# Kernel tuning notes

Hardware: AMD Instinct MI355X
Metric: run time of the kernel (lower is better)

The kernel has to match this reference:

```python
import jax, jax.numpy as jnp
import numpy as np

D, H, E, HID, TOPK = 1024, 16, 8, 2048, 2
B, L = 2, 2048

def setup_inputs() -> dict:
    key = jax.random.key(0)
    ks = jax.random.split(key, 12)
    s = 0.02
    return {
        "x": jax.random.normal(ks[0], (B, L, D), jnp.float32),
        "mask": jnp.zeros((B, L), dtype=bool),  # key_padding_mask: True = ignore
        "ln1_g": jnp.ones((D,), jnp.float32), "ln1_b": jnp.zeros((D,), jnp.float32),
        "Wqkv": jax.random.normal(ks[1], (3 * D, D), jnp.float32) * s,
        "bqkv": jnp.zeros((3 * D,), jnp.float32),
        "Wo": jax.random.normal(ks[2], (D, D), jnp.float32) * s,
        "bo": jnp.zeros((D,), jnp.float32),
        "ln2_g": jnp.ones((D,), jnp.float32), "ln2_b": jnp.zeros((D,), jnp.float32),
        "Wg": jax.random.normal(ks[3], (D, E), jnp.float32) * s,
        "bg": jnp.zeros((E,), jnp.float32),
        "W1": jax.random.normal(ks[4], (E, D, HID), jnp.float32) * s,
        "b1": jnp.zeros((E, HID), jnp.float32),
        "W2": jax.random.normal(ks[5], (E, HID, D), jnp.float32) * s,
        "b2": jnp.zeros((E, D), jnp.float32),
    }

def _layernorm(x, g, b, eps=1e-5):
    mu = x.mean(-1, keepdims=True)
    var = ((x - mu) ** 2).mean(-1, keepdims=True)
    return (x - mu) * jax.lax.rsqrt(var + eps) * g + b

def reference(x, mask, ln1_g, ln1_b, Wqkv, bqkv, Wo, bo, ln2_g, ln2_b, Wg, bg, W1, b1, W2, b2):
    b, l, d = x.shape
    dh = d // H
    # ---- pre-norm self-attention ----
    residual = x
    xn = _layernorm(x, ln1_g, ln1_b)
    qkv = xn @ Wqkv.T + bqkv                      # [B,L,3D]
    q, k, v = jnp.split(qkv, 3, axis=-1)
    q = q.reshape(b, l, H, dh).transpose(0, 2, 1, 3)  # bhld
    k = k.reshape(b, l, H, dh).transpose(0, 2, 1, 3)
    v = v.reshape(b, l, H, dh).transpose(0, 2, 1, 3)
    scores = jnp.einsum('bhqd,bhkd->bhqk', q, k) / jnp.sqrt(jnp.float32(dh))
    scores = jnp.where(mask[:, None, None, :], jnp.float32(-1e9), scores)
    attn = jax.nn.softmax(scores, axis=-1)
    ao = jnp.einsum('bhqk,bhkd->bhqd', attn, v).transpose(0, 2, 1, 3).reshape(b, l, d)
    ao = ao @ Wo.T + bo
    x = residual + ao                              # dropout is identity at eval
    # ---- pre-norm MoE FFN (top-2 softmax gating) ----
    residual = x
    xn = _layernorm(x, ln2_g, ln2_b)
    T = b * l
    xf = xn.reshape(T, d)
    probs = jax.nn.softmax(xf @ Wg + bg, axis=-1)  # [T,E]
    vals, idx = jax.lax.top_k(probs, TOPK)         # [T,K]
    wts = vals / vals.sum(-1, keepdims=True)
    # dense expert compute (reference): all experts over all tokens
    h = jax.nn.gelu(jnp.einsum('td,edh->eth', xf, W1) + b1[:, None, :], approximate=False)
    eo = jnp.einsum('eth,ehd->etd', h, W2) + b2[:, None, :]   # [E,T,D]
    sel = eo[idx, jnp.arange(T)[:, None]]          # [T,K,D]
    moe_out = (wts[..., None] * sel).sum(1).reshape(b, l, d)
    # load-balancing aux loss
    me = probs.mean(0)                             # mean gate prob per expert
    ce = jax.nn.one_hot(idx, E, dtype=probs.dtype).sum(1).mean(0)  # dispatch fraction
    moe_loss = jnp.float32(E) * jnp.sum(me * ce)
    out = residual + moe_out
    return (out, moe_loss)
```

## Files before the change

### kernel.cpp

```cpp
#include <hip/hip_runtime.h>
#include <stdint.h>

#define TOK   4096
#define DIM   1024
#define NH    16
#define DHD   64
#define NE    8
#define HIDN  2048
#define BATCH 2
#define SEQ   2048
#define BK    64

using floatx4 = __attribute__((ext_vector_type(4))) float;
using bfx8    = __attribute__((ext_vector_type(8))) __bf16;
using bfx2    = __attribute__((ext_vector_type(2))) __bf16;
using shortx8 = __attribute__((ext_vector_type(8))) short;

__device__ __forceinline__ unsigned short f2bf(float f) {
    union { __bf16 b; unsigned short u; } v;
    v.b = (__bf16)f;
    return v.u;
}

__device__ __forceinline__ unsigned pack2bf(float lo, float hi) {
    union { bfx2 v; unsigned u; } t;
    t.v[0] = (__bf16)lo;
    t.v[1] = (__bf16)hi;
    return t.u;
}

__device__ __forceinline__ floatx4 mfma16(bfx8 a, bfx8 b, floatx4 c) {
    return __builtin_amdgcn_mfma_f32_16x16x32_bf16(a, b, c, 0, 0, 0);
}

__device__ __forceinline__ void gload16(const unsigned short* g, unsigned short* l) {
    __builtin_amdgcn_global_load_lds(
        (const __attribute__((address_space(1))) unsigned int*)g,
        (__attribute__((address_space(3))) unsigned int*)l, 16, 0, 0);
}

__global__ __launch_bounds__(256) void cvt_kernel(const float* __restrict__ in,
                                                  unsigned short* __restrict__ out, int n) {
    int i = (blockIdx.x * 256 + threadIdx.x) * 4;
    if (i < n) {
        float4 v = *reinterpret_cast<const float4*>(in + i);
        out[i + 0] = f2bf(v.x);
        out[i + 1] = f2bf(v.y);
        out[i + 2] = f2bf(v.z);
        out[i + 3] = f2bf(v.w);
    }
}

__global__ __launch_bounds__(256) void transpose_cvt_kernel(const float* __restrict__ in,
                                                            unsigned short* __restrict__ out,
                                                            int R, int C) {
    __shared__ unsigned short t[64][65];
    in  += (size_t)blockIdx.z * R * C;
    out += (size_t)blockIdx.z * R * C;
    int r0 = blockIdx.y * 64, c0 = blockIdx.x * 64;
    int lr = threadIdx.x >> 4, lc = (threadIdx.x & 15) * 4;
#pragma unroll
    for (int p = 0; p < 4; p++) {
        int r = p * 16 + lr;
        float4 v = *reinterpret_cast<const float4*>(in + (size_t)(r0 + r) * C + c0 + lc);
        t[lc + 0][r] = f2bf(v.x);
        t[lc + 1][r] = f2bf(v.y);
        t[lc + 2][r] = f2bf(v.z);
        t[lc + 3][r] = f2bf(v.w);
    }
    __syncthreads();
    int c = threadIdx.x >> 2, ch = (threadIdx.x & 3) * 16;
    shortx8 o0, o1;
#pragma unroll
    for (int q = 0; q < 8; q++) { o0[q] = t[c][ch + q]; o1[q] = t[c][ch + 8 + q]; }
    unsigned short* op = out + (size_t)(c0 + c) * R + r0 + ch;
    *reinterpret_cast<shortx8*>(op) = o0;
    *reinterpret_cast<shortx8*>(op + 8) = o1;
}

__global__ __launch_bounds__(256) void kvprep_kernel(const unsigned short* __restrict__ qkv,
                                                     unsigned short* __restrict__ ktg,
                                                     unsigned short* __restrict__ vtg,
                                                     const unsigned char* __restrict__ mask,
                                                     float* __restrict__ maskf) {
    __shared__ unsigned short t[64 * 64];
    int tid = threadIdx.x;
    int s0 = blockIdx.x * 64, hd = blockIdx.y, b = blockIdx.z;
    size_t bh = (size_t)(b * NH + hd);
    if (hd == 0 && tid < 64) {
        maskf[(size_t)b * SEQ + s0 + tid] =
            mask[(size_t)b * SEQ + s0 + tid] ? -1.44269504e9f : 0.0f;
    }
#pragma unroll
    for (int i = 0; i < 2; i++) {
        int idx = i * 256 + tid;
        int sr = idx >> 3, c = idx & 7;
        shortx8 v = *reinterpret_cast<const shortx8*>(
            qkv + (size_t)(b * SEQ + s0 + sr) * 3 * DIM + DIM + hd * DHD + c * 8);
        *reinterpret_cast<shortx8*>(ktg + (bh * SEQ + s0 + sr) * DHD + c * 8) = v;
    }
#pragma unroll
    for (int i = 0; i < 2; i++) {
        int idx = i * 256 + tid;
        int sr = idx >> 3, c = idx & 7;
        shortx8 v = *reinterpret_cast<const shortx8*>(
            qkv + (size_t)(b * SEQ + s0 + sr) * 3 * DIM + 2 * DIM + hd * DHD + c * 8);
        *reinterpret_cast<shortx8*>(t + sr * 64 + ((c ^ (sr >> 3)) * 8)) = v;
    }
    __syncthreads();
#pragma unroll
    for (int i = 0; i < 2; i++) {
        int idx = i * 256 + tid;
        int d = idx >> 3, c2 = idx & 7;
        shortx8 o;
#pragma unroll
        for (int e = 0; e < 8; e++) {
            int s = c2 * 8 + e;
            o[e] = (short)t[s * 64 + (((d >> 3) ^ c2) * 8) + (d & 7)];
        }
        *reinterpret_cast<shortx8*>(vtg + (bh * DHD + d) * SEQ + s0 + c2 * 8) = o;
    }
}

__global__ __launch_bounds__(256) void ln_kernel(const float* __restrict__ x,
                                                 const float* __restrict__ g,
                                                 const float* __restrict__ b,
                                                 unsigned short* __restrict__ obf) {
    int t = blockIdx.x;
    int tid = threadIdx.x;
    const float* xr = x + (size_t)t * DIM;
    float4 v = *reinterpret_cast<const float4*>(xr + tid * 4);
    float s  = v.x + v.y + v.z + v.w;
    float s2 = v.x * v.x + v.y * v.y + v.z * v.z + v.w * v.w;
    for (int o = 32; o > 0; o >>= 1) {
        s  += __shfl_down(s,  o, 64);
        s2 += __shfl_down(s2, o, 64);
    }
    __shared__ float red[10];
    int lane = tid & 63, w = tid >> 6;
    if (lane == 0) { red[w] = s; red[4 + w] = s2; }
    __syncthreads();
    if (tid == 0) {
        float ts = red[0] + red[1] + red[2] + red[3];
        float t2 = red[4] + red[5] + red[6] + red[7];
        float mu = ts * (1.0f / DIM);
        float var = t2 * (1.0f / DIM) - mu * mu;
        red[8] = mu;
        red[9] = rsqrtf(var + 1e-5f);
    }
    __syncthreads();
    float mu = red[8], rstd = red[9];
    float4 gv = *reinterpret_cast<const float4*>(g + tid * 4);
    float4 bv = *reinterpret_cast<const float4*>(b + tid * 4);
    size_t o = (size_t)t * DIM + tid * 4;
    obf[o + 0] = f2bf((v.x - mu) * rstd * gv.x + bv.x);
    obf[o + 1] = f2bf((v.y - mu) * rstd * gv.y + bv.y);
    obf[o + 2] = f2bf((v.z - mu) * rstd * gv.z + bv.z);
    obf[o + 3] = f2bf((v.w - mu) * rstd * gv.w + bv.w);
}

template <int EPI, bool GATHER>
__global__ __launch_bounds__(256) void gemm_kernel(const unsigned short* __restrict__ A,
                                                   const unsigned short* __restrict__ Bt,
                                                   void* __restrict__ C,
                                                   const float* __restrict__ bias,
                                                   const float* __restrict__ resid,
                                                   const int* __restrict__ cnt,
                                                   const int* __restrict__ goff,
                                                   const int* __restrict__ gtok,
                                                   int M, int N, int K) {
    int e = blockIdx.z;
    int Me = cnt ? cnt[e] : M;
    int brow = blockIdx.y * 128;
    if (brow >= Me) return;
    int bcol = blockIdx.x * 128;
    int go = goff ? goff[e] : 0;
    const unsigned short* Be = Bt + (size_t)e * N * K;
    const float* biasp = bias + (size_t)e * N;

    __shared__ unsigned short As[128 * BK];
    __shared__ unsigned short Bs[128 * BK];

    int tid = threadIdx.x, lane = tid & 63, w = tid >> 6;
    int wr = w >> 1, wc = w & 1;
    int cg = lane >> 4, cl = lane & 15;

    const unsigned short* aga[4];
    const unsigned short* bga[4];
    unsigned short* asb = As + w * 2048;
    unsigned short* bsb = Bs + w * 2048;
#pragma unroll
    for (int i = 0; i < 4; i++) {
        int s = w * 256 + i * 64 + lane;
        int row = s >> 3;
        int c = (s & 7) ^ (row & 7);
        int gr = brow + row;
        if (gr >= Me) gr = Me - 1;
        long ar;
        if (GATHER) ar = gtok[go + gr];
        else if (cnt) ar = go + gr;
        else ar = gr;
        aga[i] = A + ar * (long)K + c * 8;
        bga[i] = Be + (size_t)(bcol + row) * K + c * 8;
    }

    floatx4 acc[4][4];
#pragma unroll
    for (int m = 0; m < 4; m++)
#pragma unroll
        for (int n = 0; n < 4; n++) acc[m][n] = (floatx4){0.f, 0.f, 0.f, 0.f};

    for (int kt = 0; kt < K; kt += BK) {
#pragma unroll
        for (int i = 0; i < 4; i++) {
            gload16(aga[i], asb + i * 512);
            gload16(bga[i], bsb + i * 512);
            aga[i] += BK;
            bga[i] += BK;
        }
        __syncthreads();
#pragma unroll
        for (int ks = 0; ks < 2; ks++) {
            bfx8 af[4], bf[4];
#pragma unroll
            for (int m = 0; m < 4; m++) {
                int row = wr * 64 + m * 16 + cl;
                af[m] = *reinterpret_cast<const bfx8*>(
                    As + row * BK + (((ks * 4 + cg) ^ (row & 7)) << 3));
            }
#pragma unroll
            for (int n = 0; n < 4; n++) {
                int row = wc * 64 + n * 16 + cl;
                bf[n] = *reinterpret_cast<const bfx8*>(
                    Bs + row * BK + (((ks * 4 + cg) ^ (row & 7)) << 3));
            }
#pragma unroll
            for (int m = 0; m < 4; m++)
#pragma unroll
                for (int n = 0; n < 4; n++) acc[m][n] = mfma16(af[m], bf[n], acc[m][n]);
        }
        __syncthreads();
    }

#pragma unroll
    for (int m = 0; m < 4; m++) {
#pragma unroll
        for (int j = 0; j < 4; j++) {
            int r = brow + wr * 64 + m * 16 + cg * 4 + j;
            if (r >= Me) continue;
#pragma unroll
            for (int n = 0; n < 4; n++) {
                int col = bcol + wc * 64 + n * 16 + cl;
                float v = acc[m][n][j] + biasp[col];
                if (EPI == 0) {
                    ((unsigned short*)C)[(size_t)r * N + col] = f2bf(v);
                } else if (EPI == 1) {
                    size_t o = (size_t)r * N + col;
                    ((float*)C)[o] = v + resid[o];
                } else if (EPI == 2) {
                    float gg = 0.5f * v * (1.0f + erff(v * 0.70710678f));
                    ((unsigned short*)C)[(size_t)(go + r) * N + col] = f2bf(gg);
                } else {
                    ((float*)C)[(size_t)(go + r) * N + col] = v;
                }
            }
        }
    }
}

__global__ __launch_bounds__(256) void attn_kernel(const unsigned short* __restrict__ qkv,
                                                   const unsigned short* __restrict__ ktg,
                                                   const unsigned short* __restrict__ vtg,
                                                   const float* __restrict__ maskf,
                                                   unsigned short* __restrict__ ao) {
    __shared__ unsigned short Ks[2][64 * 64];
    __shared__ unsigned short Vs[2][64 * 64];
    __shared__ unsigned short Ps[4][16 * 72];

    int tid = threadIdx.x, lane = tid & 63, w = tid >> 6;
    int cg = lane >> 4, cl = lane & 15;
    int qb = blockIdx.x * 64, hd = blockIdx.y, b = blockIdx.z;
    size_t bh = (size_t)(b * NH + hd);
    const float SC2 = 0.125f * 1.44269504f;

    int tq = qb + w * 16 + cl;
    const unsigned short* qrow = qkv + (size_t)(b * SEQ + tq) * 3 * DIM + hd * DHD;
    bfx8 aq0 = *reinterpret_cast<const bfx8*>(qrow + cg * 8);
    bfx8 aq1 = *reinterpret_cast<const bfx8*>(qrow + 32 + cg * 8);

    int srow = lane >> 3, schunk = lane & 7;
    int sg = (schunk ^ srow) * 8;
    const unsigned short* kptr = ktg + (bh * SEQ + w * 16 + srow) * DHD + sg;
    const unsigned short* vptr = vtg + (bh * DHD + w * 16 + srow) * SEQ + sg;
    const float* mrowf = maskf + (size_t)b * SEQ;
    unsigned short* psw = &Ps[w][0];
    int sw0 = (cg ^ (cl & 7)) << 3;

    floatx4 accO[4];
#pragma unroll
    for (int dt = 0; dt < 4; dt++) accO[dt] = (floatx4){0.f, 0.f, 0.f, 0.f};
    float m0 = -3.0e38f, l0 = 0.f;

    gload16(kptr, &Ks[0][w * 1024]);
    gload16(kptr + 8 * DHD, &Ks[0][w * 1024 + 512]);
    gload16(vptr, &Vs[0][w * 1024]);
    gload16(vptr + 8 * SEQ, &Vs[0][w * 1024 + 512]);
    __syncthreads();

    int cur = 0;
    for (int t = 0; t < SEQ / 64; t++) {
        if (t < SEQ / 64 - 1) {
            size_t nkt = (size_t)(t + 1) * 64;
            int nb = cur ^ 1;
            gload16(kptr + nkt * DHD, &Ks[nb][w * 1024]);
            gload16(kptr + nkt * DHD + 8 * DHD, &Ks[nb][w * 1024 + 512]);
            gload16(vptr + nkt, &Vs[nb][w * 1024]);
            gload16(vptr + nkt + 8 * SEQ, &Vs[nb][w * 1024 + 512]);
        }
        const unsigned short* ksb = &Ks[cur][0];
        const unsigned short* vsb = &Vs[cur][0];
        int kt = t * 64;

        floatx4 accS[4];
#pragma unroll
        for (int nt = 0; nt < 4; nt++) accS[nt] = (floatx4){0.f, 0.f, 0.f, 0.f};
#pragma unroll
        for (int nt = 0; nt < 4; nt++) {
            const unsigned short* kr = ksb + (nt * 16 + cl) * 64;
            bfx8 k0 = *reinterpret_cast<const bfx8*>(kr + sw0);
            bfx8 k1 = *reinterpret_cast<const bfx8*>(kr + (sw0 ^ 32));
            accS[nt] = mfma16(k0, aq0, accS[nt]);
            accS[nt] = mfma16(k1, aq1, accS[nt]);
        }

        float s[4][4];
        float tmax = -3.0e38f;
#pragma unroll
        for (int nt = 0; nt < 4; nt++) {
            float4 mk4 = *reinterpret_cast<const float4*>(mrowf + kt + nt * 16 + cg * 4);
            s[nt][0] = fmaf(accS[nt][0], SC2, mk4.x);
            s[nt][1] = fmaf(accS[nt][1], SC2, mk4.y);
            s[nt][2] = fmaf(accS[nt][2], SC2, mk4.z);
            s[nt][3] = fmaf(accS[nt][3], SC2, mk4.w);
#pragma unroll
            for (int j = 0; j < 4; j++) tmax = fmaxf(tmax, s[nt][j]);
        }
        tmax = fmaxf(tmax, __shfl_xor(tmax, 16, 64));
        tmax = fmaxf(tmax, __shfl_xor(tmax, 32, 64));

        if (!__all(tmax - m0 <= 11.5f)) {
            float mn = fmaxf(m0, tmax);
            float al = __builtin_amdgcn_exp2f(m0 - mn);
            m0 = mn;
            l0 *= al;
#pragma unroll
            for (int dt = 0; dt < 4; dt++) accO[dt] *= al;
        }

        float rs = 0.f;
        unsigned pk[4][2];
#pragma unroll
        for (int nt = 0; nt < 4; nt++) {
            float p0 = __builtin_amdgcn_exp2f(s[nt][0] - m0);
            float p1 = __builtin_amdgcn_exp2f(s[nt][1] - m0);
            float p2 = __builtin_amdgcn_exp2f(s[nt][2] - m0);
            float p3 = __builtin_amdgcn_exp2f(s[nt][3] - m0);
            rs += (p0 + p1) + (p2 + p3);
            pk[nt][0] = pack2bf(p0, p1);
            pk[nt][1] = pack2bf(p2, p3);
        }
        rs += __shfl_xor(rs, 16, 64);
        rs += __shfl_xor(rs, 32, 64);
        l0 += rs;

#pragma unroll
        for (int nt = 0; nt < 4; nt++) {
            uint2 u; u.x = pk[nt][0]; u.y = pk[nt][1];
            *reinterpret_cast<uint2*>(psw + cl * 72 + nt * 16 + cg * 4) = u;
        }
        bfx8 pf0 = *reinterpret_cast<const bfx8*>(psw + cl * 72 + cg * 8);
        bfx8 pf1 = *reinterpret_cast<const bfx8*>(psw + cl * 72 + 32 + cg * 8);
#pragma unroll
        for (int dt = 0; dt < 4; dt++) {
            const unsigned short* vr = vsb + (dt * 16 + cl) * 64;
            bfx8 v0 = *reinterpret_cast<const bfx8*>(vr + sw0);
            bfx8 v1 = *reinterpret_cast<const bfx8*>(vr + (sw0 ^ 32));
            accO[dt] = mfma16(v0, pf0, accO[dt]);
            accO[dt] = mfma16(v1, pf1, accO[dt]);
        }
        __syncthreads();
        cur ^= 1;
    }

    float rl = 1.0f / l0;
    unsigned short* aorow = ao + (size_t)(b * SEQ + qb + w * 16 + cl) * DIM + hd * DHD;
#pragma unroll
    for (int dt = 0; dt < 4; dt++) {
        uint2 u;
        u.x = pack2bf(accO[dt][0] * rl, accO[dt][1] * rl);
        u.y = pack2bf(accO[dt][2] * rl, accO[dt][3] * rl);
        *reinterpret_cast<uint2*>(aorow + dt * 16 + cg * 4) = u;
    }
}

__global__ __launch_bounds__(256) void gate_kernel(const float* __restrict__ x2,
                                                   const float* __restrict__ lng,
                                                   const float* __restrict__ lnb,
                                                   const float* __restrict__ Wg,
                                                   const float* __restrict__ bg,
                                                   unsigned short* __restrict__ xn2b,
                                                   int* __restrict__ idx,
                                                   float* __restrict__ wts,
                                                   float* __restrict__ me_part) {
    __shared__ float bme[8];
    if (threadIdx.x < 8) bme[threadIdx.x] = 0.f;
    __syncthreads();
    int w = threadIdx.x >> 6, lane = threadIdx.x & 63;
    int t = blockIdx.x * 4 + w;
    const float* xr = x2 + (size_t)t * DIM + lane * 16;
    float4 xv[4];
    float s = 0.f, s2 = 0.f;
#pragma unroll
    for (int q = 0; q < 4; q++) {
        xv[q] = *reinterpret_cast<const float4*>(xr + q * 4);
        s  += xv[q].x + xv[q].y + xv[q].z + xv[q].w;
        s2 += xv[q].x * xv[q].x + xv[q].y * xv[q].y + xv[q].z * xv[q].z + xv[q].w * xv[q].w;
    }
    for (int o = 32; o > 0; o >>= 1) {
        s  += __shfl_xor(s,  o, 64);
        s2 += __shfl_xor(s2, o, 64);
    }
    float mu = s * (1.0f / DIM);
    float rstd = rsqrtf(s2 * (1.0f / DIM) - mu * mu + 1e-5f);
    float acc[8];
#pragma unroll
    for (int e = 0; e < 8; e++) acc[e] = 0.f;
    unsigned short ob[16];
#pragma unroll
    for (int q = 0; q < 4; q++) {
        float4 gv = *reinterpret_cast<const float4*>(lng + lane * 16 + q * 4);
        float4 bv = *reinterpret_cast<const float4*>(lnb + lane * 16 + q * 4);
        float xn0 = (xv[q].x - mu) * rstd * gv.x + bv.x;
        float xn1 = (xv[q].y - mu) * rstd * gv.y + bv.y;
        float xn2 = (xv[q].z - mu) * rstd * gv.z + bv.z;
        float xn3 = (xv[q].w - mu) * rstd * gv.w + bv.w;
        ob[q * 4 + 0] = f2bf(xn0);
        ob[q * 4 + 1] = f2bf(xn1);
        ob[q * 4 + 2] = f2bf(xn2);
        ob[q * 4 + 3] = f2bf(xn3);
        const float* wr = Wg + (size_t)(lane * 16 + q * 4) * 8;
#pragma unroll
        for (int e = 0; e < 8; e++) acc[e] += xn0 * wr[e];
#pragma unroll
        for (int e = 0; e < 8; e++) acc[e] += xn1 * wr[8 + e];
#pragma unroll
        for (int e = 0; e < 8; e++) acc[e] += xn2 * wr[16 + e];
#pragma unroll
        for (int e = 0; e < 8; e++) acc[e] += xn3 * wr[24 + e];
    }
    unsigned short* op = xn2b + (size_t)t * DIM + lane * 16;
    *reinterpret_cast<shortx8*>(op)     = *reinterpret_cast<shortx8*>(&ob[0]);
    *reinterpret_cast<shortx8*>(op + 8) = *reinterpret_cast<shortx8*>(&ob[8]);
    for (int o = 32; o > 0; o >>= 1)
#pragma unroll
        for (int e = 0; e < 8; e++) acc[e] += __shfl_xor(acc[e], o, 64);
    if (lane == 0) {
        float p[8];
        float mx = -3e38f;
#pragma unroll
        for (int e = 0; e < 8; e++) { acc[e] += bg[e]; mx = fmaxf(mx, acc[e]); }
        float se = 0.f;
#pragma unroll
        for (int e = 0; e < 8; e++) { p[e] = expf(acc[e] - mx); se += p[e]; }
#pragma unroll
        for (int e = 0; e < 8; e++) p[e] /= se;
        int i0 = 0; float v0 = p[0];
#pragma unroll
        for (int e = 1; e < 8; e++) if (p[e] > v0) { v0 = p[e]; i0 = e; }
        int i1 = -1; float v1 = -3e38f;
#pragma unroll
        for (int e = 0; e < 8; e++) if (e != i0 && p[e] > v1) { v1 = p[e]; i1 = e; }
        float sw = v0 + v1;
        idx[t * 2]     = i0;
        idx[t * 2 + 1] = i1;
        wts[t * 2]     = v0 / sw;
        wts[t * 2 + 1] = v1 / sw;
#pragma unroll
        for (int e = 0; e < 8; e++) atomicAdd(&bme[e], p[e]);
    }
    __syncthreads();
    if (threadIdx.x < 8) me_part[(size_t)blockIdx.x * 8 + threadIdx.x] = bme[threadIdx.x];
}

__global__ __launch_bounds__(256) void route1_kernel(const int* __restrict__ idx,
                                                     int* __restrict__ cnt,
                                                     int* __restrict__ posl) {
    __shared__ int lh[8];
    __shared__ int gb[8];
    int tid = threadIdx.x;
    int t = blockIdx.x * 256 + tid;
    if (tid < 8) lh[tid] = 0;
    __syncthreads();
    int i0 = idx[t * 2], i1 = idx[t * 2 + 1];
    int r0 = atomicAdd(&lh[i0], 1);
    int r1 = atomicAdd(&lh[i1], 1);
    __syncthreads();
    if (tid < 8) gb[tid] = atomicAdd(&cnt[tid], lh[tid]);
    __syncthreads();
    posl[t * 2]     = gb[i0] + r0;
    posl[t * 2 + 1] = gb[i1] + r1;
}

__global__ void prefix_kernel(const int* __restrict__ cnt, int* __restrict__ goff) {
    if (threadIdx.x == 0) {
        int s = 0;
        for (int e = 0; e < 8; e++) { goff[e] = s; s += cnt[e]; }
        goff[8] = s;
    }
}

__global__ __launch_bounds__(256) void route2_kernel(const int* __restrict__ idx,
                                                     const int* __restrict__ goff,
                                                     const int* __restrict__ posl,
                                                     int* __restrict__ gtok,
                                                     int* __restrict__ tpos) {
    int t = blockIdx.x * 256 + threadIdx.x;
#pragma unroll
    for (int j = 0; j < 2; j++) {
        int e = idx[t * 2 + j];
        int p = goff[e] + posl[t * 2 + j];
        gtok[p] = t;
        tpos[t * 2 + j] = p;
    }
}

__global__ __launch_bounds__(256) void combine_kernel(const float* __restrict__ x2,
                                                      const float* __restrict__ eo,
                                                      const float* __restrict__ wts,
                                                      const int* __restrict__ tpos,
                                                      float* __restrict__ out) {
    int t = blockIdx.x;
    int c = threadIdx.x * 4;
    float w0 = wts[t * 2], w1 = wts[t * 2 + 1];
    int p0 = tpos[t * 2], p1 = tpos[t * 2 + 1];
    float4 r  = *reinterpret_cast<const float4*>(x2 + (size_t)t * DIM + c);
    float4 a  = *reinterpret_cast<const float4*>(eo + (size_t)p0 * DIM + c);
    float4 bb = *reinterpret_cast<const float4*>(eo + (size_t)p1 * DIM + c);
    float4 o;
    o.x = r.x + w0 * a.x + w1 * bb.x;
    o.y = r.y + w0 * a.y + w1 * bb.y;
    o.z = r.z + w0 * a.z + w1 * bb.z;
    o.w = r.w + w0 * a.w + w1 * bb.w;
    *reinterpret_cast<float4*>(out + (size_t)t * DIM + c) = o;
}

__global__ __launch_bounds__(256) void loss_kernel(const float* __restrict__ me_part,
                                                   const int* __restrict__ cnt,
                                                   float* __restrict__ out) {
    __shared__ float red[256];
    int tid = threadIdx.x;
    int e = tid & 7, part = tid >> 3;
    float s = 0.f;
    for (int b = part; b < 1024; b += 32) s += me_part[(size_t)b * 8 + e];
    red[tid] = s;
    __syncthreads();
    if (tid < 64) {
        float v = red[tid] + red[tid + 64] + red[tid + 128] + red[tid + 192];
        red[tid] = v;
    }
    __syncthreads();
    if (tid < 8) {
        float v = red[tid] + red[tid + 8] + red[tid + 16] + red[tid + 24] +
                  red[tid + 32] + red[tid + 40] + red[tid + 48] + red[tid + 56];
        red[tid] = v;
    }
    __syncthreads();
    if (tid == 0) {
        float s2 = 0.f;
        for (int ee = 0; ee < 8; ee++)
            s2 += (red[ee] / 4096.0f) * ((float)cnt[ee] / 4096.0f);
        out[(size_t)TOK * DIM] = 8.0f * s2;
    }
}

extern "C" void kernel_launch(void* const* d_in, const int* in_sizes, int n_in,
                              void* d_out, int out_size, void* d_ws, size_t ws_size,
                              hipStream_t stream) {
    const float* x    = (const float*)d_in[0];
    const unsigned char* mask = (const unsigned char*)d_in[1];
    const float* ln1g = (const float*)d_in[2];
    const float* ln1b = (const float*)d_in[3];
    const float* Wqkv = (const float*)d_in[4];
    const float* bqkv = (const float*)d_in[5];
    const float* Wo   = (const float*)d_in[6];
    const float* bo   = (const float*)d_in[7];
    const float* ln2g = (const float*)d_in[8];
    const float* ln2b = (const float*)d_in[9];
    const float* Wg   = (const float*)d_in[10];
    const float* bg   = (const float*)d_in[11];
    const float* W1   = (const float*)d_in[12];
    const float* b1   = (const float*)d_in[13];
    const float* W2   = (const float*)d_in[14];
    const float* b2   = (const float*)d_in[15];
    float* out = (float*)d_out;

    char* ws = (char*)d_ws;
    int*   cnt  = (int*)(ws + 0);
    int*   goff = (int*)(ws + 128);
    size_t off = 1024;
    auto alloc = [&](size_t bytes) -> void* {
        void* p = ws + off;
        off += (bytes + 255) & ~(size_t)255;
        return p;
    };
    const size_t SZ_QKVB = (size_t)TOK * 3 * DIM * 2;
    const size_t SZ_HB   = (size_t)2 * TOK * HIDN * 2;
    const size_t SZ_EOF  = (size_t)2 * TOK * DIM * 4;
    char* R1 = (char*)alloc(SZ_HB > SZ_QKVB ? SZ_HB : SZ_QKVB);
    char* R2 = (char*)alloc(SZ_EOF);
    unsigned short* qkvb  = (unsigned short*)R1;
    unsigned short* hb    = (unsigned short*)R1;
    float*          eof   = (float*)R2;
    unsigned short* xn1   = (unsigned short*)R2;
    unsigned short* aob   = (unsigned short*)(R2 + (size_t)TOK * DIM * 2);
    unsigned short* wqkvb = (unsigned short*)(R2 + (size_t)2 * TOK * DIM * 2);
    unsigned short* wob   = (unsigned short*)(R2 + (size_t)2 * TOK * DIM * 2 +
                                              (size_t)3 * DIM * DIM * 2);
    float*          x2    = (float*)alloc((size_t)TOK * DIM * 4);
    unsigned short* xn2b  = (unsigned short*)alloc((size_t)TOK * DIM * 2);
    unsigned short* w1t   = (unsigned short*)alloc((size_t)NE * DIM * HIDN * 2);
    unsigned short* w2t   = (unsigned short*)alloc((size_t)NE * DIM * HIDN * 2);
    unsigned short* ktg   = (unsigned short*)alloc((size_t)BATCH * NH * SEQ * DHD * 2);
    unsigned short* vtg   = (unsigned short*)alloc((size_t)BATCH * NH * DHD * SEQ * 2);
    float*          maskf = (float*)alloc((size_t)BATCH * SEQ * 4);
    float*          mep   = (float*)alloc((size_t)1024 * 8 * 4);
    int*            idxp  = (int*)alloc((size_t)TOK * 2 * 4);
    float*          wtsp  = (float*)alloc((size_t)TOK * 2 * 4);
    int*            posl  = (int*)alloc((size_t)TOK * 2 * 4);
    int*            gtok  = (int*)alloc((size_t)2 * TOK * 4);
    int*            tpos  = (int*)alloc((size_t)TOK * 2 * 4);

    hipMemsetAsync(ws, 0, 256, stream);

    cvt_kernel<<<3 * DIM * DIM / 1024, 256, 0, stream>>>(Wqkv, wqkvb, 3 * DIM * DIM);
    cvt_kernel<<<DIM * DIM / 1024, 256, 0, stream>>>(Wo, wob, DIM * DIM);
    transpose_cvt_kernel<<<dim3(HIDN / 64, DIM / 64, NE), 256, 0, stream>>>(W1, w1t, DIM, HIDN);
    transpose_cvt_kernel<<<dim3(DIM / 64, HIDN / 64, NE), 256, 0, stream>>>(W2, w2t, HIDN, DIM);

    ln_kernel<<<TOK, 256, 0, stream>>>(x, ln1g, ln1b, xn1);

    gemm_kernel<0, false><<<dim3(24, 32, 1), 256, 0, stream>>>(
        xn1, wqkvb, qkvb, bqkv, nullptr, nullptr, nullptr, nullptr, TOK, 3 * DIM, DIM);

    kvprep_kernel<<<dim3(SEQ / 64, NH, BATCH), 256, 0, stream>>>(qkvb, ktg, vtg, mask, maskf);

    attn_kernel<<<dim3(SEQ / 64, NH, BATCH), 256, 0, stream>>>(qkvb, ktg, vtg, maskf, aob);

    gemm_kernel<1, false><<<dim3(8, 32, 1), 256, 0, stream>>>(
        aob, wob, x2, bo, x, nullptr, nullptr, nullptr, TOK, DIM, DIM);

    gate_kernel<<<TOK / 4, 256, 0, stream>>>(x2, ln2g, ln2b, Wg, bg, xn2b,
                                             idxp, wtsp, mep);
    route1_kernel<<<TOK / 256, 256, 0, stream>>>(idxp, cnt, posl);
    prefix_kernel<<<1, 64, 0, stream>>>(cnt, goff);
    route2_kernel<<<TOK / 256, 256, 0, stream>>>(idxp, goff, posl, gtok, tpos);

    gemm_kernel<2, true><<<dim3(16, 32, 8), 256, 0, stream>>>(
        xn2b, w1t, hb, b1, nullptr, cnt, goff, gtok, TOK, HIDN, DIM);

    gemm_kernel<3, false><<<dim3(8, 32, 8), 256, 0, stream>>>(
        hb, w2t, eof, b2, nullptr, cnt, goff, nullptr, TOK, DIM, HIDN);

    combine_kernel<<<TOK, 256, 0, stream>>>(x2, eof, wtsp, tpos, out);
    loss_kernel<<<1, 256, 0, stream>>>(mep, cnt, out);
}
```

Measured before the change: 403.1 us.

## Process two query tiles per attention wave and XCD-swizzle GEMM block order

Each attention wave now handles 32 query rows (two 16-row tiles) instead of 16, so every K/V tile loaded into shared memory serves twice as many queries and the grid is halved. The softmax rescale check is evaluated per lane before the cross-lane max shuffles, so the shuffles run only when a rescale is needed. The GEMM kernel remaps its flattened block index so that consecutive logical tiles land on the same XCD, aiming for better L2 reuse. The cost is higher register pressure in attention (launch bounds now request 2 blocks per SM) and fewer attention blocks to spread across CUs.

New measurement: 366.6 us. 1.1x faster.

```diff
diff --git a/kernel.cpp b/kernel.cpp
--- a/kernel.cpp
+++ b/kernel.cpp
@@ -37,6 +37,12 @@
     __builtin_amdgcn_global_load_lds(
         (const __attribute__((address_space(1))) unsigned int*)g,
         (__attribute__((address_space(3))) unsigned int*)l, 16, 0, 0);
+}
+
+__device__ __forceinline__ int xcd_swz(int hw, int nwg) {
+    int q = nwg >> 3, r = nwg & 7;
+    int xc = hw & 7, o = hw >> 3;
+    return (xc < r ? xc * (q + 1) : r * (q + 1) + (xc - r) * q) + o;
 }
 
 __global__ __launch_bounds__(256) void cvt_kernel(const float* __restrict__ in,
@@ -169,11 +175,19 @@
                                                    const int* __restrict__ goff,
                                                    const int* __restrict__ gtok,
                                                    int M, int N, int K) {
-    int e = blockIdx.z;
+    int gx = gridDim.x, gy = gridDim.y;
+    int nwg = gx * gy * (int)gridDim.z;
+    int hw = ((int)blockIdx.z * gy + (int)blockIdx.y) * gx + (int)blockIdx.x;
+    int virt = xcd_swz(hw, nwg);
+    int bx = virt % gx;
+    int tmp = virt / gx;
+    int by = tmp % gy;
+    int e = tmp / gy;
+
     int Me = cnt ? cnt[e] : M;
-    int brow = blockIdx.y * 128;
+    int brow = by * 128;
     if (brow >= Me) return;
-    int bcol = blockIdx.x * 128;
+    int bcol = bx * 128;
     int go = goff ? goff[e] : 0;
     const unsigned short* Be = Bt + (size_t)e * N * K;
     const float* biasp = bias + (size_t)e * N;
@@ -268,38 +282,46 @@
     }
 }
 
-__global__ __launch_bounds__(256) void attn_kernel(const unsigned short* __restrict__ qkv,
-                                                   const unsigned short* __restrict__ ktg,
-                                                   const unsigned short* __restrict__ vtg,
-                                                   const float* __restrict__ maskf,
-                                                   unsigned short* __restrict__ ao) {
+__global__ __launch_bounds__(256, 2) void attn_kernel(const unsigned short* __restrict__ qkv,
+                                                      const unsigned short* __restrict__ ktg,
+                                                      const unsigned short* __restrict__ vtg,
+                                                      const float* __restrict__ maskf,
+                                                      unsigned short* __restrict__ ao) {
     __shared__ unsigned short Ks[2][64 * 64];
     __shared__ unsigned short Vs[2][64 * 64];
-    __shared__ unsigned short Ps[4][16 * 72];
+    __shared__ unsigned short Ps[4][2][16 * 72];
 
     int tid = threadIdx.x, lane = tid & 63, w = tid >> 6;
     int cg = lane >> 4, cl = lane & 15;
-    int qb = blockIdx.x * 64, hd = blockIdx.y, b = blockIdx.z;
+    int qb = blockIdx.x * 128, hd = blockIdx.y, b = blockIdx.z;
     size_t bh = (size_t)(b * NH + hd);
     const float SC2 = 0.125f * 1.44269504f;
 
-    int tq = qb + w * 16 + cl;
-    const unsigned short* qrow = qkv + (size_t)(b * SEQ + tq) * 3 * DIM + hd * DHD;
-    bfx8 aq0 = *reinterpret_cast<const bfx8*>(qrow + cg * 8);
-    bfx8 aq1 = *reinterpret_cast<const bfx8*>(qrow + 32 + cg * 8);
+    const unsigned short* qrow0 =
+        qkv + (size_t)(b * SEQ + qb + w * 32 + cl) * 3 * DIM + hd * DHD;
+    const unsigned short* qrow1 = qrow0 + (size_t)16 * 3 * DIM;
+    bfx8 aq00 = *reinterpret_cast<const bfx8*>(qrow0 + cg * 8);
+    bfx8 aq01 = *reinterpret_cast<const bfx8*>(qrow0 + 32 + cg * 8);
+    bfx8 aq10 = *reinterpret_cast<const bfx8*>(qrow1 + cg * 8);
+    bfx8 aq11 = *reinterpret_cast<const bfx8*>(qrow1 + 32 + cg * 8);
 
     int srow = lane >> 3, schunk = lane & 7;
     int sg = (schunk ^ srow) * 8;
     const unsigned short* kptr = ktg + (bh * SEQ + w * 16 + srow) * DHD + sg;
     const unsigned short* vptr = vtg + (bh * DHD + w * 16 + srow) * SEQ + sg;
     const float* mrowf = maskf + (size_t)b * SEQ;
-    unsigned short* psw = &Ps[w][0];
+    unsigned short* psw0 = &Ps[w][0][0];
+    unsigned short* psw1 = &Ps[w][1][0];
     int sw0 = (cg ^ (cl & 7)) << 3;
 
-    floatx4 accO[4];
-#pragma unroll
-    for (int dt = 0; dt < 4; dt++) accO[dt] = (floatx4){0.f, 0.f, 0.f, 0.f};
-    float m0 = -3.0e38f, l0 = 0.f;
+    floatx4 accO0[4], accO1[4];
+#pragma unroll
+    for (int dt = 0; dt < 4; dt++) {
+        accO0[dt] = (floatx4){0.f, 0.f, 0.f, 0.f};
+        accO1[dt] = (floatx4){0.f, 0.f, 0.f, 0.f};
+    }
+    float m00 = -3.0e38f, l00 = 0.f;
+    float m01 = -3.0e38f, l01 = 0.f;
 
     gload16(kptr, &Ks[0][w * 1024]);
     gload16(kptr + 8 * DHD, &Ks[0][w * 1024 + 512]);
@@ -321,85 +343,139 @@
         const unsigned short* vsb = &Vs[cur][0];
         int kt = t * 64;
 
-        floatx4 accS[4];
-#pragma unroll
-        for (int nt = 0; nt < 4; nt++) accS[nt] = (floatx4){0.f, 0.f, 0.f, 0.f};
+        floatx4 accS0[4], accS1[4];
+#pragma unroll
+        for (int nt = 0; nt < 4; nt++) {
+            accS0[nt] = (floatx4){0.f, 0.f, 0.f, 0.f};
+            accS1[nt] = (floatx4){0.f, 0.f, 0.f, 0.f};
+        }
 #pragma unroll
         for (int nt = 0; nt < 4; nt++) {
             const unsigned short* kr = ksb + (nt * 16 + cl) * 64;
             bfx8 k0 = *reinterpret_cast<const bfx8*>(kr + sw0);
             bfx8 k1 = *reinterpret_cast<const bfx8*>(kr + (sw0 ^ 32));
-            accS[nt] = mfma16(k0, aq0, accS[nt]);
-            accS[nt] = mfma16(k1, aq1, accS[nt]);
-        }
-
-        float s[4][4];
-        float tmax = -3.0e38f;
-#pragma unroll
-        for (int nt = 0; nt < 4; nt++) {
-            float4 mk4 = *reinterpret_cast<const float4*>(mrowf + kt + nt * 16 + cg * 4);
-            s[nt][0] = fmaf(accS[nt][0], SC2, mk4.x);
-            s[nt][1] = fmaf(accS[nt][1], SC2, mk4.y);
-            s[nt][2] = fmaf(accS[nt][2], SC2, mk4.z);
-            s[nt][3] = fmaf(accS[nt][3], SC2, mk4.w);
-#pragma unroll
-            for (int j = 0; j < 4; j++) tmax = fmaxf(tmax, s[nt][j]);
-        }
-        tmax = fmaxf(tmax, __shfl_xor(tmax, 16, 64));
-        tmax = fmaxf(tmax, __shfl_xor(tmax, 32, 64));
-
-        if (!__all(tmax - m0 <= 11.5f)) {
-            float mn = fmaxf(m0, tmax);
-            float al = __builtin_amdgcn_exp2f(m0 - mn);
-            m0 = mn;
-            l0 *= al;
-#pragma unroll
-            for (int dt = 0; dt < 4; dt++) accO[dt] *= al;
-        }
-
-        float rs = 0.f;
-        unsigned pk[4][2];
-#pragma unroll
-        for (int nt = 0; nt < 4; nt++) {
-            float p0 = __builtin_amdgcn_exp2f(s[nt][0] - m0);
-            float p1 = __builtin_amdgcn_exp2f(s[nt][1] - m0);
-            float p2 = __builtin_amdgcn_exp2f(s[nt][2] - m0);
-            float p3 = __builtin_amdgcn_exp2f(s[nt][3] - m0);
-            rs += (p0 + p1) + (p2 + p3);
-            pk[nt][0] = pack2bf(p0, p1);
-            pk[nt][1] = pack2bf(p2, p3);
-        }
-        rs += __shfl_xor(rs, 16, 64);
-        rs += __shfl_xor(rs, 32, 64);
-        l0 += rs;
-
-#pragma unroll
-        for (int nt = 0; nt < 4; nt++) {
-            uint2 u; u.x = pk[nt][0]; u.y = pk[nt][1];
-            *reinterpret_cast<uint2*>(psw + cl * 72 + nt * 16 + cg * 4) = u;
-        }
-        bfx8 pf0 = *reinterpret_cast<const bfx8*>(psw + cl * 72 + cg * 8);
-        bfx8 pf1 = *reinterpret_cast<const bfx8*>(psw + cl * 72 + 32 + cg * 8);
+            accS0[nt] = mfma16(k0, aq00, accS0[nt]);
+            accS0[nt] = mfma16(k1, aq01, accS0[nt]);
+            accS1[nt] = mfma16(k0, aq10, accS1[nt]);
+            accS1[nt] = mfma16(k1, aq11, accS1[nt]);
+        }
+
+        float4 mk[4];
+#pragma unroll
+        for (int nt = 0; nt < 4; nt++)
+            mk[nt] = *reinterpret_cast<const float4*>(mrowf + kt + nt * 16 + cg * 4);
+
+        {
+            float s[4][4];
+            float tmax = -3.0e38f;
+#pragma unroll
+            for (int nt = 0; nt < 4; nt++) {
+                s[nt][0] = fmaf(accS0[nt][0], SC2, mk[nt].x);
+                s[nt][1] = fmaf(accS0[nt][1], SC2, mk[nt].y);
+                s[nt][2] = fmaf(accS0[nt][2], SC2, mk[nt].z);
+                s[nt][3] = fmaf(accS0[nt][3], SC2, mk[nt].w);
+#pragma unroll
+                for (int j = 0; j < 4; j++) tmax = fmaxf(tmax, s[nt][j]);
+            }
+            if (!__all(tmax - m00 <= 11.5f)) {
+                tmax = fmaxf(tmax, __shfl_xor(tmax, 16, 64));
+                tmax = fmaxf(tmax, __shfl_xor(tmax, 32, 64));
+                float mn = fmaxf(m00, tmax);
+                float al = __builtin_amdgcn_exp2f(m00 - mn);
+                m00 = mn;
+                l00 *= al;
+#pragma unroll
+                for (int dt = 0; dt < 4; dt++) accO0[dt] *= al;
+            }
+            float rs = 0.f;
+#pragma unroll
+            for (int nt = 0; nt < 4; nt++) {
+                float p0 = __builtin_amdgcn_exp2f(s[nt][0] - m00);
+                float p1 = __builtin_amdgcn_exp2f(s[nt][1] - m00);
+                float p2 = __builtin_amdgcn_exp2f(s[nt][2] - m00);
+                float p3 = __builtin_amdgcn_exp2f(s[nt][3] - m00);
+                rs += (p0 + p1) + (p2 + p3);
+                uint2 u;
+                u.x = pack2bf(p0, p1);
+                u.y = pack2bf(p2, p3);
+                *reinterpret_cast<uint2*>(psw0 + cl * 72 + nt * 16 + cg * 4) = u;
+            }
+            rs += __shfl_xor(rs, 16, 64);
+            rs += __shfl_xor(rs, 32, 64);
+            l00 += rs;
+        }
+        {
+            float s[4][4];
+            float tmax = -3.0e38f;
+#pragma unroll
+            for (int nt = 0; nt < 4; nt++) {
+                s[nt][0] = fmaf(accS1[nt][0], SC2, mk[nt].x);
+                s[nt][1] = fmaf(accS1[nt][1], SC2, mk[nt].y);
+                s[nt][2] = fmaf(accS1[nt][2], SC2, mk[nt].z);
+                s[nt][3] = fmaf(accS1[nt][3], SC2, mk[nt].w);
+#pragma unroll
+                for (int j = 0; j < 4; j++) tmax = fmaxf(tmax, s[nt][j]);
+            }
+            if (!__all(tmax - m01 <= 11.5f)) {
+                tmax = fmaxf(tmax, __shfl_xor(tmax, 16, 64));
+                tmax = fmaxf(tmax, __shfl_xor(tmax, 32, 64));
+                float mn = fmaxf(m01, tmax);
+                float al = __builtin_amdgcn_exp2f(m01 - mn);
+                m01 = mn;
+                l01 *= al;
+#pragma unroll
+                for (int dt = 0; dt < 4; dt++) accO1[dt] *= al;
+            }
+            float rs = 0.f;
+#pragma unroll
+            for (int nt = 0; nt < 4; nt++) {
+                float p0 = __builtin_amdgcn_exp2f(s[nt][0] - m01);
+                float p1 = __builtin_amdgcn_exp2f(s[nt][1] - m01);
+                float p2 = __builtin_amdgcn_exp2f(s[nt][2] - m01);
+                float p3 = __builtin_amdgcn_exp2f(s[nt][3] - m01);
+                rs += (p0 + p1) + (p2 + p3);
+                uint2 u;
+                u.x = pack2bf(p0, p1);
+                u.y = pack2bf(p2, p3);
+                *reinterpret_cast<uint2*>(psw1 + cl * 72 + nt * 16 + cg * 4) = u;
+            }
+            rs += __shfl_xor(rs, 16, 64);
+            rs += __shfl_xor(rs, 32, 64);
+            l01 += rs;
+        }
+
+        bfx8 pf00 = *reinterpret_cast<const bfx8*>(psw0 + cl * 72 + cg * 8);
+        bfx8 pf01 = *reinterpret_cast<const bfx8*>(psw0 + cl * 72 + 32 + cg * 8);
+        bfx8 pf10 = *reinterpret_cast<const bfx8*>(psw1 + cl * 72 + cg * 8);
+        bfx8 pf11 = *reinterpret_cast<const bfx8*>(psw1 + cl * 72 + 32 + cg * 8);
 #pragma unroll
         for (int dt = 0; dt < 4; dt++) {
             const unsigned short* vr = vsb + (dt * 16 + cl) * 64;
             bfx8 v0 = *reinterpret_cast<const bfx8*>(vr + sw0);
             bfx8 v1 = *reinterpret_cast<const bfx8*>(vr + (sw0 ^ 32));
-            accO[dt] = mfma16(v0, pf0, accO[dt]);
-            accO[dt] = mfma16(v1, pf1, accO[dt]);
+            accO0[dt] = mfma16(v0, pf00, accO0[dt]);
+            accO0[dt] = mfma16(v1, pf01, accO0[dt]);
+            accO1[dt] = mfma16(v0, pf10, accO1[dt]);
+            accO1[dt] = mfma16(v1, pf11, accO1[dt]);
         }
         __syncthreads();
         cur ^= 1;
     }
 
-    float rl = 1.0f / l0;
-    unsigned short* aorow = ao + (size_t)(b * SEQ + qb + w * 16 + cl) * DIM + hd * DHD;
+    float rl0 = 1.0f / l00;
+    float rl1 = 1.0f / l01;
+    unsigned short* aorow0 =
+        ao + (size_t)(b * SEQ + qb + w * 32 + cl) * DIM + hd * DHD;
+    unsigned short* aorow1 = aorow0 + (size_t)16 * DIM;
 #pragma unroll
     for (int dt = 0; dt < 4; dt++) {
         uint2 u;
-        u.x = pack2bf(accO[dt][0] * rl, accO[dt][1] * rl);
-        u.y = pack2bf(accO[dt][2] * rl, accO[dt][3] * rl);
-        *reinterpret_cast<uint2*>(aorow + dt * 16 + cg * 4) = u;
+        u.x = pack2bf(accO0[dt][0] * rl0, accO0[dt][1] * rl0);
+        u.y = pack2bf(accO0[dt][2] * rl0, accO0[dt][3] * rl0);
+        *reinterpret_cast<uint2*>(aorow0 + dt * 16 + cg * 4) = u;
+        u.x = pack2bf(accO1[dt][0] * rl1, accO1[dt][1] * rl1);
+        u.y = pack2bf(accO1[dt][2] * rl1, accO1[dt][3] * rl1);
+        *reinterpret_cast<uint2*>(aorow1 + dt * 16 + cg * 4) = u;
     }
 }
 
@@ -654,7 +730,7 @@
 
     kvprep_kernel<<<dim3(SEQ / 64, NH, BATCH), 256, 0, stream>>>(qkvb, ktg, vtg, mask, maskf);
 
-    attn_kernel<<<dim3(SEQ / 64, NH, BATCH), 256, 0, stream>>>(qkvb, ktg, vtg, maskf, aob);
+    attn_kernel<<<dim3(SEQ / 128, NH, BATCH), 256, 0, stream>>>(qkvb, ktg, vtg, maskf, aob);
 
     gemm_kernel<1, false><<<dim3(8, 32, 1), 256, 0, stream>>>(
         aob, wob, x2, bo, x, nullptr, nullptr, nullptr, TOK, DIM, DIM);
```
